# Optimization experiments

Hardware: AMD Instinct MI355X
Metric: run time of the kernel (lower is better)

The kernel has to match this reference:

```python
import jax, jax.numpy as jnp
import numpy as np

NUM_HEADS = 32
NUM_KV_HEADS = 4
HEAD_DIM = 128
HIDDEN = 4096
Q_HID = NUM_HEADS * HEAD_DIM        # 4096
KV_HID = NUM_KV_HEADS * HEAD_DIM    # 512
TOTAL = Q_HID + 2 * KV_HID          # 5120
T = 16384                            # total tokens (batch*seq, flattened)
EPS = 1e-6


def setup_inputs() -> dict:
    key = jax.random.key(0)
    k1, k2, k3, k4 = jax.random.split(key, 4)
    hidden_states = jax.random.normal(k1, (T, HIDDEN), dtype=jnp.float32)
    # per-token sin/cos in duplicated-half (neox) layout, shape [T, HEAD_DIM]
    angles = jax.random.uniform(k2, (T, HEAD_DIM // 2), dtype=jnp.float32) * 6.283
    sin = jnp.concatenate([jnp.sin(angles), jnp.sin(angles)], axis=-1)
    cos = jnp.concatenate([jnp.cos(angles), jnp.cos(angles)], axis=-1)
    w_qkv = jax.random.normal(k3, (TOTAL, HIDDEN), dtype=jnp.float32) * 0.02
    q_norm_w = jnp.ones((HEAD_DIM,), dtype=jnp.float32) + 0.1 * jax.random.normal(k4, (HEAD_DIM,), dtype=jnp.float32)
    k_norm_w = jnp.ones((HEAD_DIM,), dtype=jnp.float32)
    return {"hidden_states": hidden_states, "sin": sin, "cos": cos,
            "w_qkv": w_qkv, "q_norm_w": q_norm_w, "k_norm_w": k_norm_w}


def _rmsnorm_rope(x, w, sin, cos):
    # x: [T, H, D]; per-head RMSNorm in fp32 then rotate-half RoPE
    var = jnp.mean(x * x, axis=-1, keepdims=True)          # [T, H, 1]
    xn = x * jax.lax.rsqrt(var + EPS) * w                   # [T, H, D]
    half = HEAD_DIM // 2
    x1, x2 = xn[..., :half], xn[..., half:]
    rot = jnp.concatenate([-x2, x1], axis=-1)               # rotate_half
    s = sin[:, None, :]
    c = cos[:, None, :]
    return rot * s + xn * c


def reference(hidden_states, sin, cos, w_qkv, q_norm_w, k_norm_w):
    # fused QKV projection
    qkv = jnp.einsum('td,ed->te', hidden_states, w_qkv)     # [T, 5120]
    q = qkv[:, :Q_HID].reshape(-1, NUM_HEADS, HEAD_DIM)
    k = qkv[:, Q_HID:Q_HID + KV_HID].reshape(-1, NUM_KV_HEADS, HEAD_DIM)
    v = qkv[:, Q_HID + KV_HID:]                              # plain copy, no norm/rope
    q = _rmsnorm_rope(q, q_norm_w, sin, cos).reshape(-1, Q_HID)
    k = _rmsnorm_rope(k, k_norm_w, sin, cos).reshape(-1, KV_HID)
    return jnp.concatenate([q, k, v], axis=-1)               # [T, 5120]
```

## Files before the change

### kernel.cpp

```cpp
#include <hip/hip_runtime.h>
#include <hip/hip_bf16.h>

#define T_TOK   16384
#define HID     4096
#define NTOT    5120
#define Q_HID   4096
#define KV_END  4608
#define HD      128
#define EPSV    1e-6f

typedef __bf16 bf16x8 __attribute__((ext_vector_type(8)));
typedef float  f32x4  __attribute__((ext_vector_type(4)));

__device__ __forceinline__ unsigned short f2bf(float f) {
    unsigned u = __builtin_bit_cast(unsigned, f);
    u += 0x7fffu + ((u >> 16) & 1u);
    return (unsigned short)(u >> 16);
}

__global__ void cvt_bf16(const float* __restrict__ in,
                         unsigned short* __restrict__ out, long n) {
    long i = 4L * (blockIdx.x * (long)blockDim.x + threadIdx.x);
    if (i >= n) return;
    float4 v = *reinterpret_cast<const float4*>(in + i);
    ushort4 o;
    o.x = f2bf(v.x); o.y = f2bf(v.y); o.z = f2bf(v.z); o.w = f2bf(v.w);
    *reinterpret_cast<ushort4*>(out + i) = o;
}

#define BM 128
#define BN 128
#define BK 32

__global__ __launch_bounds__(256)
void gemm_rmsnorm_rope(const unsigned short* __restrict__ A,
                       const unsigned short* __restrict__ B,
                       const float* __restrict__ sinp,
                       const float* __restrict__ cosp,
                       const float* __restrict__ qw,
                       const float* __restrict__ kw,
                       float* __restrict__ out)
{
    __shared__ unsigned short sA[BM * BK];
    __shared__ unsigned short sB[BN * BK];

    const int tid  = threadIdx.x;
    const int wave = tid >> 6;
    const int lane = tid & 63;
    const int l15  = lane & 15;
    const int quad = lane >> 4;

    const int m0 = blockIdx.y * BM;
    const int n0 = blockIdx.x * BN;

    const unsigned short* Ab = A + (size_t)m0 * HID;
    const unsigned short* Bb = B + (size_t)n0 * HID;

    f32x4 acc[2][8];
    const f32x4 zero = {0.f, 0.f, 0.f, 0.f};
#pragma unroll
    for (int tm = 0; tm < 2; ++tm)
#pragma unroll
        for (int tn = 0; tn < 8; ++tn) acc[tm][tn] = zero;

    const unsigned short* aAddr[2];
    const unsigned short* bAddr[8];
#pragma unroll
    for (int tm = 0; tm < 2; ++tm)
        aAddr[tm] = sA + (wave * 32 + tm * 16 + l15) * BK + quad * 8;
#pragma unroll
    for (int tn = 0; tn < 8; ++tn)
        bAddr[tn] = sB + (tn * 16 + l15) * BK + quad * 8;

    for (int k0 = 0; k0 < HID; k0 += BK) {
        __syncthreads();
#pragma unroll
        for (int it = 0; it < 2; ++it) {
            const int chunk = tid + it * 256;
            const int row = chunk >> 2;
            const int kp  = chunk & 3;
            const unsigned short* gA = Ab + (size_t)row * HID + k0 + kp * 8;
            const unsigned short* gB = Bb + (size_t)row * HID + k0 + kp * 8;
            __builtin_amdgcn_global_load_lds(
                (const __attribute__((address_space(1))) void*)gA,
                (__attribute__((address_space(3))) void*)(sA + chunk * 8),
                16, 0, 0);
            __builtin_amdgcn_global_load_lds(
                (const __attribute__((address_space(1))) void*)gB,
                (__attribute__((address_space(3))) void*)(sB + chunk * 8),
                16, 0, 0);
        }
        __syncthreads();

        bf16x8 af[2], bf[8];
#pragma unroll
        for (int tm = 0; tm < 2; ++tm)
            af[tm] = *reinterpret_cast<const bf16x8*>(aAddr[tm]);
#pragma unroll
        for (int tn = 0; tn < 8; ++tn)
            bf[tn] = *reinterpret_cast<const bf16x8*>(bAddr[tn]);

#pragma unroll
        for (int tm = 0; tm < 2; ++tm)
#pragma unroll
            for (int tn = 0; tn < 8; ++tn)
                acc[tm][tn] = __builtin_amdgcn_mfma_f32_16x16x32_bf16(
                    af[tm], bf[tn], acc[tm][tn], 0, 0, 0);
    }

    if (n0 >= KV_END) {
#pragma unroll
        for (int tm = 0; tm < 2; ++tm)
#pragma unroll
            for (int r = 0; r < 4; ++r) {
                const int row = m0 + wave * 32 + tm * 16 + quad * 4 + r;
                float* orow = out + (size_t)row * NTOT + n0;
#pragma unroll
                for (int tn = 0; tn < 8; ++tn)
                    orow[tn * 16 + l15] = acc[tm][tn][r];
            }
    } else {
        const float* w = (n0 < Q_HID) ? qw : kw;
        float wv[8];
#pragma unroll
        for (int tn = 0; tn < 8; ++tn) wv[tn] = w[tn * 16 + l15];

#pragma unroll
        for (int tm = 0; tm < 2; ++tm)
#pragma unroll
            for (int r = 0; r < 4; ++r) {
                const int row = m0 + wave * 32 + tm * 16 + quad * 4 + r;
                float ss = 0.f;
#pragma unroll
                for (int tn = 0; tn < 8; ++tn) {
                    const float v = acc[tm][tn][r];
                    ss += v * v;
                }
                ss += __shfl_xor(ss, 1);
                ss += __shfl_xor(ss, 2);
                ss += __shfl_xor(ss, 4);
                ss += __shfl_xor(ss, 8);
                const float scale = rsqrtf(ss * (1.0f / 128.0f) + EPSV);

                float xn[8];
#pragma unroll
                for (int tn = 0; tn < 8; ++tn)
                    xn[tn] = acc[tm][tn][r] * scale * wv[tn];

                const float* srow = sinp + (size_t)row * HD;
                const float* crow = cosp + (size_t)row * HD;
                float* orow = out + (size_t)row * NTOT + n0;
#pragma unroll
                for (int tn = 0; tn < 4; ++tn) {
                    const int c = tn * 16 + l15;
                    const float sv = srow[c];
                    const float cv = crow[c];
                    orow[c]      = xn[tn] * cv - xn[tn + 4] * sv;
                    orow[c + 64] = xn[tn] * sv + xn[tn + 4] * cv;
                }
            }
    }
}

extern "C" void kernel_launch(void* const* d_in, const int* in_sizes, int n_in,
                              void* d_out, int out_size, void* d_ws, size_t ws_size,
                              hipStream_t stream) {
    const float* hidden = (const float*)d_in[0];
    const float* sinp   = (const float*)d_in[1];
    const float* cosp   = (const float*)d_in[2];
    const float* w_qkv  = (const float*)d_in[3];
    const float* qnw    = (const float*)d_in[4];
    const float* knw    = (const float*)d_in[5];
    float* out = (float*)d_out;

    unsigned short* Abf = (unsigned short*)d_ws;
    unsigned short* Bbf = Abf + (size_t)T_TOK * HID;

    const long nA = (long)T_TOK * HID;
    const long nB = (long)NTOT * HID;
    cvt_bf16<<<(unsigned)(nA / 4 / 256), 256, 0, stream>>>(hidden, Abf, nA);
    cvt_bf16<<<(unsigned)(nB / 4 / 256), 256, 0, stream>>>(w_qkv, Bbf, nB);

    dim3 grid(NTOT / BN, T_TOK / BM);
    gemm_rmsnorm_rope<<<grid, 256, 0, stream>>>(Abf, Bbf, sinp, cosp, qnw, knw, out);
}
```

Baseline: 1.547 ms.

## Rewrite GEMM with 256x256 tiles, double-buffered swizzled LDS and phased MFMA schedule

Replaces the 128x128x32 single-buffered GEMM with a 256x256x64 tile using 512 threads and double-buffered LDS filled by async global_load_lds. The LDS layout is XOR-swizzled to avoid bank conflicts. Compute is split into barrier-separated phases with s_setprio so the next tile's loads overlap MFMAs. A grid-stride cvt kernel and an XCD-aware block remap are also added. The kernel now needs 128KB of dynamic LDS, which allows only one block per CU, and relies on hand-tuned vmcnt waits.

```diff
diff --git a/kernel.cpp b/kernel.cpp
--- a/kernel.cpp
+++ b/kernel.cpp
@@ -9,6 +9,12 @@
 #define HD      128
 #define EPSV    1e-6f
 
+#define BM 256
+#define BN 256
+#define BK 64
+#define NT (HID / BK)
+#define THREADS 512
+
 typedef __bf16 bf16x8 __attribute__((ext_vector_type(8)));
 typedef float  f32x4  __attribute__((ext_vector_type(4)));
 
@@ -18,21 +24,101 @@
     return (unsigned short)(u >> 16);
 }
 
-__global__ void cvt_bf16(const float* __restrict__ in,
-                         unsigned short* __restrict__ out, long n) {
-    long i = 4L * (blockIdx.x * (long)blockDim.x + threadIdx.x);
-    if (i >= n) return;
-    float4 v = *reinterpret_cast<const float4*>(in + i);
-    ushort4 o;
-    o.x = f2bf(v.x); o.y = f2bf(v.y); o.z = f2bf(v.z); o.w = f2bf(v.w);
-    *reinterpret_cast<ushort4*>(out + i) = o;
-}
-
-#define BM 128
-#define BN 128
-#define BK 32
-
 __global__ __launch_bounds__(256)
+void cvt_bf16(const float* __restrict__ in, unsigned short* __restrict__ out,
+              long n) {
+    const long stride = (long)gridDim.x * blockDim.x * 8;
+    for (long base = 8L * (blockIdx.x * (long)blockDim.x + threadIdx.x);
+         base < n; base += stride) {
+        float4 v0 = *reinterpret_cast<const float4*>(in + base);
+        float4 v1 = *reinterpret_cast<const float4*>(in + base + 4);
+        ushort4 o0, o1;
+        o0.x = f2bf(v0.x); o0.y = f2bf(v0.y); o0.z = f2bf(v0.z); o0.w = f2bf(v0.w);
+        o1.x = f2bf(v1.x); o1.y = f2bf(v1.y); o1.z = f2bf(v1.z); o1.w = f2bf(v1.w);
+        *reinterpret_cast<ushort4*>(out + base)     = o0;
+        *reinterpret_cast<ushort4*>(out + base + 4) = o1;
+    }
+}
+
+#define PH_BARRIER() asm volatile("s_barrier" ::: "memory")
+
+#define STAGE(SAP, SBP, KT) do {                                              \
+    const int _ko = (KT) * BK;                                                \
+    _Pragma("unroll")                                                         \
+    for (int s = 0; s < 4; ++s) {                                             \
+        __builtin_amdgcn_global_load_lds(                                     \
+            (const __attribute__((address_space(1))) void*)(Ab + off[s] + _ko),\
+            (__attribute__((address_space(3))) void*)((SAP) + dst + s * 4096), \
+            16, 0, 0);                                                        \
+        __builtin_amdgcn_global_load_lds(                                     \
+            (const __attribute__((address_space(1))) void*)(Bb + off[s] + _ko),\
+            (__attribute__((address_space(3))) void*)((SBP) + dst + s * 4096), \
+            16, 0, 0);                                                        \
+    }                                                                         \
+} while (0)
+
+#define KTILE(SAP, SBP, TT) do {                                              \
+    const char* const Al_ = (const char*)(SAP);                               \
+    const char* const Bl_ = (const char*)(SBP);                               \
+    bf16x8 af[4][2], bfz[4][2];                                               \
+                   \
+    _Pragma("unroll") for (int mf = 0; mf < 2; ++mf)                          \
+    _Pragma("unroll") for (int ks = 0; ks < 2; ++ks)                          \
+        af[mf][ks] = *(const bf16x8*)(Al_ + aBase[ks] + mf * 2048);           \
+    _Pragma("unroll") for (int nf = 0; nf < 4; ++nf)                          \
+    _Pragma("unroll") for (int ks = 0; ks < 2; ++ks)                          \
+        bfz[nf][ks] = *(const bf16x8*)(Bl_ + bBase[ks] + nf * 2048);          \
+    PH_BARRIER();                                                             \
+    __builtin_amdgcn_s_setprio(1);                                            \
+    _Pragma("unroll") for (int mf = 0; mf < 2; ++mf)                          \
+    _Pragma("unroll") for (int nf = 0; nf < 4; ++nf)                          \
+    _Pragma("unroll") for (int ks = 0; ks < 2; ++ks)                          \
+        acc[mf][nf] = __builtin_amdgcn_mfma_f32_16x16x32_bf16(                \
+            af[mf][ks], bfz[nf][ks], acc[mf][nf], 0, 0, 0);                   \
+    __builtin_amdgcn_s_setprio(0);                                            \
+    PH_BARRIER();                                                             \
+                                \
+    _Pragma("unroll") for (int mf = 2; mf < 4; ++mf)                          \
+    _Pragma("unroll") for (int ks = 0; ks < 2; ++ks)                          \
+        af[mf][ks] = *(const bf16x8*)(Al_ + aBase[ks] + mf * 2048);           \
+    PH_BARRIER();                                                             \
+    __builtin_amdgcn_s_setprio(1);                                            \
+    _Pragma("unroll") for (int mf = 2; mf < 4; ++mf)                          \
+    _Pragma("unroll") for (int nf = 0; nf < 4; ++nf)                          \
+    _Pragma("unroll") for (int ks = 0; ks < 2; ++ks)                          \
+        acc[mf][nf] = __builtin_amdgcn_mfma_f32_16x16x32_bf16(                \
+            af[mf][ks], bfz[nf][ks], acc[mf][nf], 0, 0, 0);                   \
+    __builtin_amdgcn_s_setprio(0);                                            \
+    PH_BARRIER();                                                             \
+                                \
+    _Pragma("unroll") for (int nf = 0; nf < 4; ++nf)                          \
+    _Pragma("unroll") for (int ks = 0; ks < 2; ++ks)                          \
+        bfz[nf][ks] = *(const bf16x8*)(Bl_ + bBase[ks] + (nf + 4) * 2048);    \
+    PH_BARRIER();                                                             \
+    __builtin_amdgcn_s_setprio(1);                                            \
+    _Pragma("unroll") for (int mf = 0; mf < 2; ++mf)                          \
+    _Pragma("unroll") for (int nf = 0; nf < 4; ++nf)                          \
+    _Pragma("unroll") for (int ks = 0; ks < 2; ++ks)                          \
+        acc[mf][nf + 4] = __builtin_amdgcn_mfma_f32_16x16x32_bf16(            \
+            af[mf][ks], bfz[nf][ks], acc[mf][nf + 4], 0, 0, 0);               \
+    __builtin_amdgcn_s_setprio(0);                                            \
+    PH_BARRIER();                                                             \
+        \
+    if ((TT) + 2 < NT) STAGE(SAP, SBP, (TT) + 2);                             \
+    PH_BARRIER();                                                             \
+    __builtin_amdgcn_s_setprio(1);                                            \
+    _Pragma("unroll") for (int mf = 2; mf < 4; ++mf)                          \
+    _Pragma("unroll") for (int nf = 0; nf < 4; ++nf)                          \
+    _Pragma("unroll") for (int ks = 0; ks < 2; ++ks)                          \
+        acc[mf][nf + 4] = __builtin_amdgcn_mfma_f32_16x16x32_bf16(            \
+            af[mf][ks], bfz[nf][ks], acc[mf][nf + 4], 0, 0, 0);               \
+    __builtin_amdgcn_s_setprio(0);                                            \
+    if ((TT) + 2 < NT) { asm volatile("s_waitcnt vmcnt(8)" ::: "memory"); }   \
+    else               { asm volatile("s_waitcnt vmcnt(0)" ::: "memory"); }   \
+    PH_BARRIER();                                                             \
+} while (0)
+
+__global__ __launch_bounds__(THREADS)
 void gemm_rmsnorm_rope(const unsigned short* __restrict__ A,
                        const unsigned short* __restrict__ B,
                        const float* __restrict__ sinp,
@@ -41,99 +127,93 @@
                        const float* __restrict__ kw,
                        float* __restrict__ out)
 {
-    __shared__ unsigned short sA[BM * BK];
-    __shared__ unsigned short sB[BN * BK];
+    extern __shared__ unsigned short smem[];
+    unsigned short* const sA0 = smem;
+    unsigned short* const sA1 = smem + 16384;
+    unsigned short* const sB0 = smem + 32768;
+    unsigned short* const sB1 = smem + 49152;
 
     const int tid  = threadIdx.x;
-    const int wave = tid >> 6;
+    const int wid  = tid >> 6;
     const int lane = tid & 63;
     const int l15  = lane & 15;
     const int quad = lane >> 4;
-
-    const int m0 = blockIdx.y * BM;
-    const int n0 = blockIdx.x * BN;
-
-    const unsigned short* Ab = A + (size_t)m0 * HID;
-    const unsigned short* Bb = B + (size_t)n0 * HID;
-
-    f32x4 acc[2][8];
+    const int wr   = wid >> 1;
+    const int wc   = wid & 1;
+
+    const int bid = blockIdx.x;
+    const int wg  = (bid & 7) * 160 + (bid >> 3);
+    const int bx  = wg % 20;
+    const int by  = wg / 20;
+    const int m0  = by * BM;
+    const int n0  = bx * BN;
+
+    const unsigned short* __restrict__ Ab = A + (size_t)m0 * HID;
+    const unsigned short* __restrict__ Bb = B + (size_t)n0 * HID;
+
+    int off[4];
+#pragma unroll
+    for (int s = 0; s < 4; ++s) {
+        const int chunk = tid + s * THREADS;
+        const int row   = chunk >> 3;
+        const int slotp = (chunk & 7) ^ (row & 7);
+        off[s] = row * HID + slotp * 8;
+    }
+    const int dst = tid * 8;
+
+    int aBase[2], bBase[2];
+#pragma unroll
+    for (int ks = 0; ks < 2; ++ks) {
+        const int sl = (((ks << 2) | quad) ^ (l15 & 7)) * 16;
+        aBase[ks] = (wr * 64  + l15) * 128 + sl;
+        bBase[ks] = (wc * 128 + l15) * 128 + sl;
+    }
+
+    f32x4 acc[4][8];
     const f32x4 zero = {0.f, 0.f, 0.f, 0.f};
 #pragma unroll
-    for (int tm = 0; tm < 2; ++tm)
-#pragma unroll
-        for (int tn = 0; tn < 8; ++tn) acc[tm][tn] = zero;
-
-    const unsigned short* aAddr[2];
-    const unsigned short* bAddr[8];
-#pragma unroll
-    for (int tm = 0; tm < 2; ++tm)
-        aAddr[tm] = sA + (wave * 32 + tm * 16 + l15) * BK + quad * 8;
-#pragma unroll
-    for (int tn = 0; tn < 8; ++tn)
-        bAddr[tn] = sB + (tn * 16 + l15) * BK + quad * 8;
-
-    for (int k0 = 0; k0 < HID; k0 += BK) {
-        __syncthreads();
-#pragma unroll
-        for (int it = 0; it < 2; ++it) {
-            const int chunk = tid + it * 256;
-            const int row = chunk >> 2;
-            const int kp  = chunk & 3;
-            const unsigned short* gA = Ab + (size_t)row * HID + k0 + kp * 8;
-            const unsigned short* gB = Bb + (size_t)row * HID + k0 + kp * 8;
-            __builtin_amdgcn_global_load_lds(
-                (const __attribute__((address_space(1))) void*)gA,
-                (__attribute__((address_space(3))) void*)(sA + chunk * 8),
-                16, 0, 0);
-            __builtin_amdgcn_global_load_lds(
-                (const __attribute__((address_space(1))) void*)gB,
-                (__attribute__((address_space(3))) void*)(sB + chunk * 8),
-                16, 0, 0);
-        }
-        __syncthreads();
-
-        bf16x8 af[2], bf[8];
-#pragma unroll
-        for (int tm = 0; tm < 2; ++tm)
-            af[tm] = *reinterpret_cast<const bf16x8*>(aAddr[tm]);
-#pragma unroll
-        for (int tn = 0; tn < 8; ++tn)
-            bf[tn] = *reinterpret_cast<const bf16x8*>(bAddr[tn]);
-
-#pragma unroll
-        for (int tm = 0; tm < 2; ++tm)
-#pragma unroll
-            for (int tn = 0; tn < 8; ++tn)
-                acc[tm][tn] = __builtin_amdgcn_mfma_f32_16x16x32_bf16(
-                    af[tm], bf[tn], acc[tm][tn], 0, 0, 0);
-    }
-
-    if (n0 >= KV_END) {
-#pragma unroll
-        for (int tm = 0; tm < 2; ++tm)
+    for (int mf = 0; mf < 4; ++mf)
+#pragma unroll
+        for (int nf = 0; nf < 8; ++nf) acc[mf][nf] = zero;
+
+    STAGE(sA0, sB0, 0);
+    STAGE(sA1, sB1, 1);
+    asm volatile("s_waitcnt vmcnt(8)" ::: "memory");
+    PH_BARRIER();
+
+    for (int t = 0; t < NT; t += 2) {
+        KTILE(sA0, sB0, t);
+        KTILE(sA1, sB1, t + 1);
+    }
+
+    const int n0w   = n0 + wc * 128;
+    const int rbase = m0 + wr * 64;
+    if (n0w >= KV_END) {
+#pragma unroll
+        for (int mf = 0; mf < 4; ++mf)
 #pragma unroll
             for (int r = 0; r < 4; ++r) {
-                const int row = m0 + wave * 32 + tm * 16 + quad * 4 + r;
-                float* orow = out + (size_t)row * NTOT + n0;
-#pragma unroll
-                for (int tn = 0; tn < 8; ++tn)
-                    orow[tn * 16 + l15] = acc[tm][tn][r];
+                const int row = rbase + mf * 16 + quad * 4 + r;
+                float* orow = out + (size_t)row * NTOT + n0w;
+#pragma unroll
+                for (int nf = 0; nf < 8; ++nf)
+                    orow[nf * 16 + l15] = acc[mf][nf][r];
             }
     } else {
-        const float* w = (n0 < Q_HID) ? qw : kw;
+        const float* w = (n0w < Q_HID) ? qw : kw;
         float wv[8];
 #pragma unroll
-        for (int tn = 0; tn < 8; ++tn) wv[tn] = w[tn * 16 + l15];
-
-#pragma unroll
-        for (int tm = 0; tm < 2; ++tm)
+        for (int nf = 0; nf < 8; ++nf) wv[nf] = w[nf * 16 + l15];
+
+#pragma unroll
+        for (int mf = 0; mf < 4; ++mf)
 #pragma unroll
             for (int r = 0; r < 4; ++r) {
-                const int row = m0 + wave * 32 + tm * 16 + quad * 4 + r;
+                const int row = rbase + mf * 16 + quad * 4 + r;
                 float ss = 0.f;
 #pragma unroll
-                for (int tn = 0; tn < 8; ++tn) {
-                    const float v = acc[tm][tn][r];
+                for (int nf = 0; nf < 8; ++nf) {
+                    const float v = acc[mf][nf][r];
                     ss += v * v;
                 }
                 ss += __shfl_xor(ss, 1);
@@ -144,19 +224,19 @@
 
                 float xn[8];
 #pragma unroll
-                for (int tn = 0; tn < 8; ++tn)
-                    xn[tn] = acc[tm][tn][r] * scale * wv[tn];
+                for (int nf = 0; nf < 8; ++nf)
+                    xn[nf] = acc[mf][nf][r] * scale * wv[nf];
 
                 const float* srow = sinp + (size_t)row * HD;
                 const float* crow = cosp + (size_t)row * HD;
-                float* orow = out + (size_t)row * NTOT + n0;
-#pragma unroll
-                for (int tn = 0; tn < 4; ++tn) {
-                    const int c = tn * 16 + l15;
+                float* orow = out + (size_t)row * NTOT + n0w;
+#pragma unroll
+                for (int nf = 0; nf < 4; ++nf) {
+                    const int c = nf * 16 + l15;
                     const float sv = srow[c];
                     const float cv = crow[c];
-                    orow[c]      = xn[tn] * cv - xn[tn + 4] * sv;
-                    orow[c + 64] = xn[tn] * sv + xn[tn + 4] * cv;
+                    orow[c]      = xn[nf] * cv - xn[nf + 4] * sv;
+                    orow[c + 64] = xn[nf] * sv + xn[nf + 4] * cv;
                 }
             }
     }
@@ -178,9 +258,12 @@
 
     const long nA = (long)T_TOK * HID;
     const long nB = (long)NTOT * HID;
-    cvt_bf16<<<(unsigned)(nA / 4 / 256), 256, 0, stream>>>(hidden, Abf, nA);
-    cvt_bf16<<<(unsigned)(nB / 4 / 256), 256, 0, stream>>>(w_qkv, Bbf, nB);
-
-    dim3 grid(NTOT / BN, T_TOK / BM);
-    gemm_rmsnorm_rope<<<grid, 256, 0, stream>>>(Abf, Bbf, sinp, cosp, qnw, knw, out);
-}
+    cvt_bf16<<<2048, 256, 0, stream>>>(hidden, Abf, nA);
+    cvt_bf16<<<1024, 256, 0, stream>>>(w_qkv, Bbf, nB);
+
+    hipFuncSetAttribute(reinterpret_cast<const void*>(gemm_rmsnorm_rope),
+                        hipFuncAttributeMaxDynamicSharedMemorySize, 131072);
+
+    gemm_rmsnorm_rope<<<1280, THREADS, 131072, stream>>>(
+        Abf, Bbf, sinp, cosp, qnw, knw, out);
+}
```

Result: faster. 1.245 ms (-19.5%).
